# Performance work log

Measured on AMD Instinct MI355X. Metric: run time of the kernel, lower is better.

## Reference

```python
import jax, jax.numpy as jnp
import numpy as np

EPS = 1e-8  # torch.nn.CosineSimilarity default eps

def setup_inputs() -> dict:
    key = jax.random.key(0)
    k1, k2 = jax.random.split(key)
    B, R, T, D = 256, 36, 64, 1024
    img_feats = jax.random.normal(k1, (B, R, D), dtype=jnp.float32)
    cap_feats = jax.random.normal(k2, (B, T, D), dtype=jnp.float32)
    cap_mask = jnp.ones((B, T), dtype=jnp.float32)  # unused by the original forward
    return {"img_feats": img_feats, "cap_feats": cap_feats, "cap_mask": cap_mask}

def reference(img_feats, cap_feats, cap_mask):
    # img_feats: (B, R, D); cap_feats: (B, T, D)
    # cosine similarity between every region r and every caption word t:
    # scores[b, r, t] = (img[b,r] . cap[b,t]) / max(||img[b,r]|| * ||cap[b,t]||, eps)
    dots = jnp.einsum('brd,btd->brt', img_feats, cap_feats)
    img_norm = jnp.linalg.norm(img_feats, axis=-1)  # (B, R)
    cap_norm = jnp.linalg.norm(cap_feats, axis=-1)  # (B, T)
    denom = jnp.maximum(img_norm[:, :, None] * cap_norm[:, None, :], EPS)
    scores = dots / denom  # (B, R, T)
    # softmax over regions (dim=1 in the original)
    attn = jax.nn.softmax(scores, axis=1)  # (B, R, T)
    # weighted sum over regions -> per-word image representation (B, T, D)
    img_cap_reps = jnp.einsum('brt,brd->btd', attn, img_feats)
    return img_cap_reps
```

## Files before the change

### kernel.cpp

```cpp
#include <hip/hip_runtime.h>
#include <hip/hip_bf16.h>

#define DDIM 1024
#define RREG 36
#define TTOK 64
#define KPAD 48

typedef __attribute__((ext_vector_type(4))) float f32x4;
typedef __attribute__((ext_vector_type(8))) short bf16x8;

__device__ __forceinline__ float sq4(float4 v) {
  return v.x * v.x + v.y * v.y + v.z * v.z + v.w * v.w;
}

__device__ __forceinline__ bf16x8 cvt8(float4 a, float4 b) {
  union { bf16x8 v; __hip_bfloat162 h[4]; } u;
  u.h[0] = __float22bfloat162_rn(make_float2(a.x, a.y));
  u.h[1] = __float22bfloat162_rn(make_float2(a.z, a.w));
  u.h[2] = __float22bfloat162_rn(make_float2(b.x, b.y));
  u.h[3] = __float22bfloat162_rn(make_float2(b.z, b.w));
  return u.v;
}

__device__ __forceinline__ bf16x8 pack8(const float* v) {
  union { bf16x8 x; __hip_bfloat162 h[4]; } u;
#pragma unroll
  for (int i = 0; i < 4; ++i)
    u.h[i] = __float22bfloat162_rn(make_float2(v[2 * i], v[2 * i + 1]));
  return u.x;
}

__device__ __forceinline__ unsigned short f2bf(float x) {
  unsigned int u = __float_as_uint(x);
  u += 0x7fffu + ((u >> 16) & 1u);
  return (unsigned short)(u >> 16);
}

__global__ __launch_bounds__(192) void scan_attn(
    const float* __restrict__ img, const float* __restrict__ cap,
    unsigned short* __restrict__ attnw) {
  __shared__ float sdots[16][52];
  __shared__ float sni[KPAD];
  __shared__ float snc[16];

  const int tid  = threadIdx.x;
  const int lane = tid & 63;
  const int wave = tid >> 6;
  const int fm   = lane & 15;
  const int kq   = lane >> 4;
  const int b    = blockIdx.x >> 2;
  const int t0   = (blockIdx.x & 3) << 4;

  const float* capb = cap + (size_t)b * TTOK * DDIM;
  const float* imgb = img + (size_t)b * RREG * DDIM;

  const int t = t0 + fm;
  const int r = wave * 16 + fm;
  const bool rv = (r < RREG);

  const float* aptr = capb + t * DDIM + kq * 8;
  const float* bptr = imgb + (rv ? r : 0) * DDIM + kq * 8;

  f32x4 acc0 = {0.f, 0.f, 0.f, 0.f}, acc1 = {0.f, 0.f, 0.f, 0.f};
  float cn = 0.f, inrm = 0.f;

#pragma unroll 2
  for (int kc = 0; kc < 16; ++kc) {
    float4 a0 = *(const float4*)(aptr);
    float4 a1 = *(const float4*)(aptr + 4);
    float4 a2 = *(const float4*)(aptr + 32);
    float4 a3 = *(const float4*)(aptr + 36);
    float4 b0 = make_float4(0.f, 0.f, 0.f, 0.f), b1 = b0, b2 = b0, b3 = b0;
    if (rv) {
      b0 = *(const float4*)(bptr);
      b1 = *(const float4*)(bptr + 4);
      b2 = *(const float4*)(bptr + 32);
      b3 = *(const float4*)(bptr + 36);
    }
    aptr += 64; bptr += 64;
    cn   += sq4(a0) + sq4(a1) + sq4(a2) + sq4(a3);
    inrm += sq4(b0) + sq4(b1) + sq4(b2) + sq4(b3);
    acc0 = __builtin_amdgcn_mfma_f32_16x16x32_bf16(cvt8(a0, a1), cvt8(b0, b1), acc0, 0, 0, 0);
    acc1 = __builtin_amdgcn_mfma_f32_16x16x32_bf16(cvt8(a2, a3), cvt8(b2, b3), acc1, 0, 0, 0);
  }
  acc0 += acc1;

  cn   += __shfl_xor(cn, 16);   cn   += __shfl_xor(cn, 32);
  inrm += __shfl_xor(inrm, 16); inrm += __shfl_xor(inrm, 32);
  if (lane < 16) {
    sni[wave * 16 + fm] = sqrtf(inrm);
    if (wave == 0) snc[fm] = sqrtf(cn);
  }
#pragma unroll
  for (int i = 0; i < 4; ++i)
    sdots[kq * 4 + i][wave * 16 + fm] = acc0[i];
  __syncthreads();

  if (tid < 16) {
    const float cnv = snc[tid];
    float sc[RREG];
    float mx = -1e30f;
#pragma unroll
    for (int rr = 0; rr < RREG; ++rr) {
      float dnm = fmaxf(sni[rr] * cnv, 1e-8f);
      float v = sdots[tid][rr] / dnm;
      sc[rr] = v;
      mx = fmaxf(mx, v);
    }
    float sum = 0.f;
#pragma unroll
    for (int rr = 0; rr < RREG; ++rr) {
      float ev = __expf(sc[rr] - mx);
      sc[rr] = ev;
      sum += ev;
    }
    const float rinv = 1.f / sum;
    unsigned short* arow = attnw + ((size_t)b * TTOK + t0 + tid) * KPAD;
#pragma unroll
    for (int r0 = 0; r0 < RREG; r0 += 4) {
      ushort4 p;
      p.x = f2bf(sc[r0 + 0] * rinv);
      p.y = f2bf(sc[r0 + 1] * rinv);
      p.z = f2bf(sc[r0 + 2] * rinv);
      p.w = f2bf(sc[r0 + 3] * rinv);
      *(ushort4*)(arow + r0) = p;
    }
    ushort4 zz; zz.x = 0; zz.y = 0; zz.z = 0; zz.w = 0;
    *(ushort4*)(arow + 36) = zz;
    *(ushort4*)(arow + 40) = zz;
    *(ushort4*)(arow + 44) = zz;
  }
}

__global__ __launch_bounds__(256) void scan_out(
    const float* __restrict__ img, const unsigned short* __restrict__ attnw,
    float* __restrict__ out) {
  const int tid  = threadIdx.x;
  const int lane = tid & 63;
  const int wave = tid >> 6;
  const int fm   = lane & 15;
  const int kq   = lane >> 4;
  const int b    = blockIdx.x >> 2;
  const int d0   = (blockIdx.x & 3) << 8;

  const float* imgb = img + (size_t)b * RREG * DDIM;
  const unsigned short* attb = attnw + (size_t)b * TTOK * KPAD;
  float* outb = out + (size_t)b * TTOK * DDIM;

  const unsigned short* ap = attb + (wave * 16 + fm) * KPAD;
  bf16x8 zf = {0, 0, 0, 0, 0, 0, 0, 0};
  bf16x8 af0 = *(const bf16x8*)(ap + kq * 8);
  bf16x8 af1 = zf;
  if (kq < 2) af1 = *(const bf16x8*)(ap + 32 + kq * 8);

  for (int s = 0; s < 16; ++s) {
    const int d = d0 + s * 16 + fm;
    float v[8];
#pragma unroll
    for (int j = 0; j < 8; ++j) v[j] = imgb[(kq * 8 + j) * DDIM + d];
    bf16x8 bf0 = pack8(v);
    bf16x8 bf1 = zf;
    if (kq == 0) {
      float w[8];
#pragma unroll
      for (int j = 0; j < 4; ++j) w[j] = imgb[(32 + j) * DDIM + d];
#pragma unroll
      for (int j = 4; j < 8; ++j) w[j] = 0.f;
      bf1 = pack8(w);
    }
    f32x4 o = {0.f, 0.f, 0.f, 0.f};
    o = __builtin_amdgcn_mfma_f32_16x16x32_bf16(af0, bf0, o, 0, 0, 0);
    o = __builtin_amdgcn_mfma_f32_16x16x32_bf16(af1, bf1, o, 0, 0, 0);
    float* op = outb + (wave * 16 + kq * 4) * DDIM + d;
#pragma unroll
    for (int i = 0; i < 4; ++i) op[i * DDIM] = o[i];
  }
}

extern "C" void kernel_launch(void* const* d_in, const int* in_sizes, int n_in,
                              void* d_out, int out_size, void* d_ws, size_t ws_size,
                              hipStream_t stream) {
  const float* img = (const float*)d_in[0];
  const float* cap = (const float*)d_in[1];
  float* out = (float*)d_out;
  unsigned short* attnw = (unsigned short*)d_ws;

  scan_attn<<<dim3(1024), dim3(192), 0, stream>>>(img, cap, attnw);
  scan_out<<<dim3(1024), dim3(256), 0, stream>>>(img, attnw, out);
}
```

Measured before the change: 178.9 us.

## Stage cap and img chunks as bf16 in LDS before MFMA in scan_attn

The dot-product kernel now uses 256 threads that cooperatively load 256-column chunks of the 16 caption rows and 36 image rows as float4, convert them to bf16, and store them in padded shared memory. The first three waves then run MFMAs from LDS. Before, each lane streamed strided global loads directly into MFMA operands, which gave poor coalescing and had the padded image rows issue predicated loads. The new scheme adds LDS traffic and two barriers per chunk, and leaves one wave idle during the MFMA phase.

```diff
diff --git a/kernel.cpp b/kernel.cpp
--- a/kernel.cpp
+++ b/kernel.cpp
@@ -5,6 +5,8 @@
 #define RREG 36
 #define TTOK 64
 #define KPAD 48
+#define CHUNK 256
+#define LSTR 264
 
 typedef __attribute__((ext_vector_type(4))) float f32x4;
 typedef __attribute__((ext_vector_type(8))) short bf16x8;
@@ -13,13 +15,11 @@
   return v.x * v.x + v.y * v.y + v.z * v.z + v.w * v.w;
 }
 
-__device__ __forceinline__ bf16x8 cvt8(float4 a, float4 b) {
-  union { bf16x8 v; __hip_bfloat162 h[4]; } u;
-  u.h[0] = __float22bfloat162_rn(make_float2(a.x, a.y));
-  u.h[1] = __float22bfloat162_rn(make_float2(a.z, a.w));
-  u.h[2] = __float22bfloat162_rn(make_float2(b.x, b.y));
-  u.h[3] = __float22bfloat162_rn(make_float2(b.z, b.w));
-  return u.v;
+__device__ __forceinline__ ushort4 cvt4(float4 v) {
+  union { ushort4 u; __hip_bfloat162 h[2]; } r;
+  r.h[0] = __float22bfloat162_rn(make_float2(v.x, v.y));
+  r.h[1] = __float22bfloat162_rn(make_float2(v.z, v.w));
+  return r.u;
 }
 
 __device__ __forceinline__ bf16x8 pack8(const float* v) {
@@ -36,9 +36,11 @@
   return (unsigned short)(u >> 16);
 }
 
-__global__ __launch_bounds__(192) void scan_attn(
+__global__ __launch_bounds__(256) void scan_attn(
     const float* __restrict__ img, const float* __restrict__ cap,
     unsigned short* __restrict__ attnw) {
+  __shared__ unsigned short scap[16 * LSTR];
+  __shared__ unsigned short simg[48 * LSTR];
   __shared__ float sdots[16][52];
   __shared__ float sni[KPAD];
   __shared__ float snc[16];
@@ -54,46 +56,58 @@
   const float* capb = cap + (size_t)b * TTOK * DDIM;
   const float* imgb = img + (size_t)b * RREG * DDIM;
 
-  const int t = t0 + fm;
-  const int r = wave * 16 + fm;
-  const bool rv = (r < RREG);
-
-  const float* aptr = capb + t * DDIM + kq * 8;
-  const float* bptr = imgb + (rv ? r : 0) * DDIM + kq * 8;
-
-  f32x4 acc0 = {0.f, 0.f, 0.f, 0.f}, acc1 = {0.f, 0.f, 0.f, 0.f};
-  float cn = 0.f, inrm = 0.f;
-
-#pragma unroll 2
-  for (int kc = 0; kc < 16; ++kc) {
-    float4 a0 = *(const float4*)(aptr);
-    float4 a1 = *(const float4*)(aptr + 4);
-    float4 a2 = *(const float4*)(aptr + 32);
-    float4 a3 = *(const float4*)(aptr + 36);
-    float4 b0 = make_float4(0.f, 0.f, 0.f, 0.f), b1 = b0, b2 = b0, b3 = b0;
-    if (rv) {
-      b0 = *(const float4*)(bptr);
-      b1 = *(const float4*)(bptr + 4);
-      b2 = *(const float4*)(bptr + 32);
-      b3 = *(const float4*)(bptr + 36);
-    }
-    aptr += 64; bptr += 64;
-    cn   += sq4(a0) + sq4(a1) + sq4(a2) + sq4(a3);
-    inrm += sq4(b0) + sq4(b1) + sq4(b2) + sq4(b3);
-    acc0 = __builtin_amdgcn_mfma_f32_16x16x32_bf16(cvt8(a0, a1), cvt8(b0, b1), acc0, 0, 0, 0);
-    acc1 = __builtin_amdgcn_mfma_f32_16x16x32_bf16(cvt8(a2, a3), cvt8(b2, b3), acc1, 0, 0, 0);
-  }
-  acc0 += acc1;
-
-  cn   += __shfl_xor(cn, 16);   cn   += __shfl_xor(cn, 32);
-  inrm += __shfl_xor(inrm, 16); inrm += __shfl_xor(inrm, 32);
-  if (lane < 16) {
-    sni[wave * 16 + fm] = sqrtf(inrm);
-    if (wave == 0) snc[fm] = sqrtf(cn);
-  }
-#pragma unroll
-  for (int i = 0; i < 4; ++i)
-    sdots[kq * 4 + i][wave * 16 + fm] = acc0[i];
+  {
+    ushort4 zz; zz.x = 0; zz.y = 0; zz.z = 0; zz.w = 0;
+    for (int i = tid; i < 792; i += 256)
+      *(ushort4*)(simg + 36 * LSTR + i * 4) = zz;
+  }
+
+  const int u = tid >> 2;
+  const int q = tid & 3;
+  const bool active = (u < 52);
+  const bool is_cap = (u < 16);
+  const float* srcrow = is_cap ? (capb + (size_t)(t0 + u) * DDIM)
+                               : (imgb + (size_t)(active ? (u - 16) : 0) * DDIM);
+  unsigned short* dstrow = is_cap ? (scap + u * LSTR) : (simg + (u - 16) * LSTR);
+
+  float nrm = 0.f;
+  f32x4 acc = {0.f, 0.f, 0.f, 0.f};
+
+  for (int c = 0; c < 4; ++c) {
+    if (c) __syncthreads();
+    if (active) {
+#pragma unroll
+      for (int s = 0; s < 16; ++s) {
+        const int col = s * 16 + q * 4;
+        float4 v = *(const float4*)(srcrow + c * CHUNK + col);
+        nrm += sq4(v);
+        *(ushort4*)(dstrow + col) = cvt4(v);
+      }
+    }
+    __syncthreads();
+    if (wave < 3) {
+      const unsigned short* arow = scap + fm * LSTR + kq * 8;
+      const unsigned short* brow = simg + (wave * 16 + fm) * LSTR + kq * 8;
+#pragma unroll
+      for (int ks = 0; ks < 8; ++ks) {
+        bf16x8 av = *(const bf16x8*)(arow + ks * 32);
+        bf16x8 bv = *(const bf16x8*)(brow + ks * 32);
+        acc = __builtin_amdgcn_mfma_f32_16x16x32_bf16(av, bv, acc, 0, 0, 0);
+      }
+    }
+  }
+
+  nrm += __shfl_xor(nrm, 1);
+  nrm += __shfl_xor(nrm, 2);
+  if (active && q == 0) {
+    if (is_cap) snc[u] = sqrtf(nrm);
+    else        sni[u - 16] = sqrtf(nrm);
+  }
+  if (wave < 3) {
+#pragma unroll
+    for (int i = 0; i < 4; ++i)
+      sdots[kq * 4 + i][wave * 16 + fm] = acc[i];
+  }
   __syncthreads();
 
   if (tid < 16) {
@@ -185,6 +199,6 @@
   float* out = (float*)d_out;
   unsigned short* attnw = (unsigned short*)d_ws;
 
-  scan_attn<<<dim3(1024), dim3(192), 0, stream>>>(img, cap, attnw);
+  scan_attn<<<dim3(1024), dim3(256), 0, stream>>>(img, cap, attnw);
   scan_out<<<dim3(1024), dim3(256), 0, stream>>>(img, attnw, out);
 }
```

After: 170.1 us. 4.9% less time.

## Restructure scan_attn to one block per batch with split-K across eight waves

Applied to the files above, without the earlier changes.

The attention kernel now processes a whole batch per 512-thread block. Each of eight waves computes all 64x36 dot products over its own 128-wide slice of D and handles the full token and region tiles. Partial results are reduced through shared memory, and norms are reduced across waves. This removes the reloading of img rows by four separate blocks and the redundant cap and img norm computations, and it raises per-wave MFMA work. In exchange the grid shrinks to 256 blocks, shared memory use grows to about 53KB, and register pressure from 12 accumulators rises.

```diff
diff --git a/kernel.cpp b/kernel.cpp
--- a/kernel.cpp
+++ b/kernel.cpp
@@ -5,6 +5,7 @@
 #define RREG 36
 #define TTOK 64
 #define KPAD 48
+#define SLOTSTR 49
 
 typedef __attribute__((ext_vector_type(4))) float f32x4;
 typedef __attribute__((ext_vector_type(8))) short bf16x8;
@@ -36,86 +37,162 @@
   return (unsigned short)(u >> 16);
 }
 
-__global__ __launch_bounds__(192) void scan_attn(
+__global__ __launch_bounds__(512) void scan_attn(
     const float* __restrict__ img, const float* __restrict__ cap,
     unsigned short* __restrict__ attnw) {
-  __shared__ float sdots[16][52];
-  __shared__ float sni[KPAD];
-  __shared__ float snc[16];
+  __shared__ __align__(16) unsigned char smem[53760];
+  float* pdots = (float*)smem;
+  float* snc_p = (float*)(smem + 50176);
+  float* sni_p = (float*)(smem + 52224);
 
   const int tid  = threadIdx.x;
   const int lane = tid & 63;
-  const int wave = tid >> 6;
+  const int w    = tid >> 6;
   const int fm   = lane & 15;
   const int kq   = lane >> 4;
-  const int b    = blockIdx.x >> 2;
-  const int t0   = (blockIdx.x & 3) << 4;
+  const int b    = blockIdx.x;
 
   const float* capb = cap + (size_t)b * TTOK * DDIM;
   const float* imgb = img + (size_t)b * RREG * DDIM;
 
-  const int t = t0 + fm;
-  const int r = wave * 16 + fm;
-  const bool rv = (r < RREG);
-
-  const float* aptr = capb + t * DDIM + kq * 8;
-  const float* bptr = imgb + (rv ? r : 0) * DDIM + kq * 8;
-
-  f32x4 acc0 = {0.f, 0.f, 0.f, 0.f}, acc1 = {0.f, 0.f, 0.f, 0.f};
-  float cn = 0.f, inrm = 0.f;
-
-#pragma unroll 2
-  for (int kc = 0; kc < 16; ++kc) {
-    float4 a0 = *(const float4*)(aptr);
-    float4 a1 = *(const float4*)(aptr + 4);
-    float4 a2 = *(const float4*)(aptr + 32);
-    float4 a3 = *(const float4*)(aptr + 36);
-    float4 b0 = make_float4(0.f, 0.f, 0.f, 0.f), b1 = b0, b2 = b0, b3 = b0;
-    if (rv) {
-      b0 = *(const float4*)(bptr);
-      b1 = *(const float4*)(bptr + 4);
-      b2 = *(const float4*)(bptr + 32);
-      b3 = *(const float4*)(bptr + 36);
-    }
-    aptr += 64; bptr += 64;
-    cn   += sq4(a0) + sq4(a1) + sq4(a2) + sq4(a3);
-    inrm += sq4(b0) + sq4(b1) + sq4(b2) + sq4(b3);
-    acc0 = __builtin_amdgcn_mfma_f32_16x16x32_bf16(cvt8(a0, a1), cvt8(b0, b1), acc0, 0, 0, 0);
-    acc1 = __builtin_amdgcn_mfma_f32_16x16x32_bf16(cvt8(a2, a3), cvt8(b2, b3), acc1, 0, 0, 0);
-  }
-  acc0 += acc1;
-
-  cn   += __shfl_xor(cn, 16);   cn   += __shfl_xor(cn, 32);
-  inrm += __shfl_xor(inrm, 16); inrm += __shfl_xor(inrm, 32);
+  const float* capk = capb + w * 128 + kq * 8;
+  const float* imgk = imgb + w * 128 + kq * 8;
+
+  f32x4 acc[4][3];
+#pragma unroll
+  for (int tt = 0; tt < 4; ++tt)
+#pragma unroll
+    for (int rt = 0; rt < 3; ++rt) acc[tt][rt] = (f32x4){0.f, 0.f, 0.f, 0.f};
+  float cnp[4] = {0.f, 0.f, 0.f, 0.f};
+  float inp[3] = {0.f, 0.f, 0.f};
+
+  const int  r2  = 32 + fm;
+  const bool r2v = (r2 < RREG);
+
+#pragma unroll
+  for (int ks = 0; ks < 4; ++ks) {
+    const int ko = ks * 32;
+    float4 a0[4], a1[4];
+#pragma unroll
+    for (int tt = 0; tt < 4; ++tt) {
+      const float* p = capk + (tt * 16 + fm) * DDIM + ko;
+      a0[tt] = *(const float4*)p;
+      a1[tt] = *(const float4*)(p + 4);
+    }
+    float4 b0[3], b1[3];
+#pragma unroll
+    for (int rt = 0; rt < 2; ++rt) {
+      const float* p = imgk + (rt * 16 + fm) * DDIM + ko;
+      b0[rt] = *(const float4*)p;
+      b1[rt] = *(const float4*)(p + 4);
+    }
+    {
+      const float* p = imgk + (r2v ? r2 : 0) * DDIM + ko;
+      float4 t0 = *(const float4*)p;
+      float4 t1 = *(const float4*)(p + 4);
+      if (!r2v) { t0 = make_float4(0.f, 0.f, 0.f, 0.f); t1 = t0; }
+      b0[2] = t0; b1[2] = t1;
+    }
+#pragma unroll
+    for (int tt = 0; tt < 4; ++tt) cnp[tt] += sq4(a0[tt]) + sq4(a1[tt]);
+#pragma unroll
+    for (int rt = 0; rt < 3; ++rt) inp[rt] += sq4(b0[rt]) + sq4(b1[rt]);
+    bf16x8 af[4], bfv[3];
+#pragma unroll
+    for (int tt = 0; tt < 4; ++tt) af[tt] = cvt8(a0[tt], a1[tt]);
+#pragma unroll
+    for (int rt = 0; rt < 3; ++rt) bfv[rt] = cvt8(b0[rt], b1[rt]);
+#pragma unroll
+    for (int tt = 0; tt < 4; ++tt)
+#pragma unroll
+      for (int rt = 0; rt < 3; ++rt)
+        acc[tt][rt] = __builtin_amdgcn_mfma_f32_16x16x32_bf16(af[tt], bfv[rt], acc[tt][rt], 0, 0, 0);
+  }
+
+#pragma unroll
+  for (int tt = 0; tt < 4; ++tt) {
+    cnp[tt] += __shfl_xor(cnp[tt], 16);
+    cnp[tt] += __shfl_xor(cnp[tt], 32);
+  }
+#pragma unroll
+  for (int rt = 0; rt < 3; ++rt) {
+    inp[rt] += __shfl_xor(inp[rt], 16);
+    inp[rt] += __shfl_xor(inp[rt], 32);
+  }
   if (lane < 16) {
-    sni[wave * 16 + fm] = sqrtf(inrm);
-    if (wave == 0) snc[fm] = sqrtf(cn);
-  }
-#pragma unroll
-  for (int i = 0; i < 4; ++i)
-    sdots[kq * 4 + i][wave * 16 + fm] = acc0[i];
+#pragma unroll
+    for (int tt = 0; tt < 4; ++tt) snc_p[w * 64 + tt * 16 + lane] = cnp[tt];
+#pragma unroll
+    for (int rt = 0; rt < 3; ++rt) {
+      int r = rt * 16 + lane;
+      if (r < RREG) sni_p[w * 48 + r] = inp[rt];
+    }
+  }
+
+  float* slot = pdots + (w & 3) * (TTOK * SLOTSTR);
+  if (w < 4) {
+#pragma unroll
+    for (int tt = 0; tt < 4; ++tt)
+#pragma unroll
+      for (int rt = 0; rt < 3; ++rt)
+#pragma unroll
+        for (int i = 0; i < 4; ++i)
+          slot[(tt * 16 + kq * 4 + i) * SLOTSTR + rt * 16 + fm] = acc[tt][rt][i];
+  }
   __syncthreads();
-
-  if (tid < 16) {
-    const float cnv = snc[tid];
+  if (w >= 4) {
+#pragma unroll
+    for (int tt = 0; tt < 4; ++tt)
+#pragma unroll
+      for (int rt = 0; rt < 3; ++rt)
+#pragma unroll
+        for (int i = 0; i < 4; ++i) {
+          int idx = (tt * 16 + kq * 4 + i) * SLOTSTR + rt * 16 + fm;
+          slot[idx] += acc[tt][rt][i];
+        }
+  }
+  __syncthreads();
+
+  if (tid < 64) {
+    float s = 0.f;
+#pragma unroll
+    for (int w2 = 0; w2 < 8; ++w2) s += snc_p[w2 * 64 + tid];
+    snc_p[tid] = sqrtf(s);
+  } else if (tid < 112) {
+    int r = tid - 64;
+    if (r < RREG) {
+      float s = 0.f;
+#pragma unroll
+      for (int w2 = 0; w2 < 8; ++w2) s += sni_p[w2 * 48 + r];
+      sni_p[r] = sqrtf(s);
+    }
+  }
+  __syncthreads();
+
+  if (w < 4 && lane < 16) {
+    const int t = w * 16 + lane;
+    const float nc = snc_p[t];
     float sc[RREG];
     float mx = -1e30f;
 #pragma unroll
-    for (int rr = 0; rr < RREG; ++rr) {
-      float dnm = fmaxf(sni[rr] * cnv, 1e-8f);
-      float v = sdots[tid][rr] / dnm;
-      sc[rr] = v;
+    for (int r = 0; r < RREG; ++r) {
+      float d = pdots[t * SLOTSTR + r] +
+                pdots[TTOK * SLOTSTR + t * SLOTSTR + r] +
+                pdots[2 * TTOK * SLOTSTR + t * SLOTSTR + r] +
+                pdots[3 * TTOK * SLOTSTR + t * SLOTSTR + r];
+      float v = d / fmaxf(sni_p[r] * nc, 1e-8f);
+      sc[r] = v;
       mx = fmaxf(mx, v);
     }
     float sum = 0.f;
 #pragma unroll
-    for (int rr = 0; rr < RREG; ++rr) {
-      float ev = __expf(sc[rr] - mx);
-      sc[rr] = ev;
+    for (int r = 0; r < RREG; ++r) {
+      float ev = __expf(sc[r] - mx);
+      sc[r] = ev;
       sum += ev;
     }
     const float rinv = 1.f / sum;
-    unsigned short* arow = attnw + ((size_t)b * TTOK + t0 + tid) * KPAD;
+    unsigned short* arow = attnw + ((size_t)b * TTOK + t) * KPAD;
 #pragma unroll
     for (int r0 = 0; r0 < RREG; r0 += 4) {
       ushort4 p;
@@ -161,12 +238,12 @@
     bf16x8 bf0 = pack8(v);
     bf16x8 bf1 = zf;
     if (kq == 0) {
-      float w[8];
-#pragma unroll
-      for (int j = 0; j < 4; ++j) w[j] = imgb[(32 + j) * DDIM + d];
-#pragma unroll
-      for (int j = 4; j < 8; ++j) w[j] = 0.f;
-      bf1 = pack8(w);
+      float wv[8];
+#pragma unroll
+      for (int j = 0; j < 4; ++j) wv[j] = imgb[(32 + j) * DDIM + d];
+#pragma unroll
+      for (int j = 4; j < 8; ++j) wv[j] = 0.f;
+      bf1 = pack8(wv);
     }
     f32x4 o = {0.f, 0.f, 0.f, 0.f};
     o = __builtin_amdgcn_mfma_f32_16x16x32_bf16(af0, bf0, o, 0, 0, 0);
@@ -185,6 +262,6 @@
   float* out = (float*)d_out;
   unsigned short* attnw = (unsigned short*)d_ws;
 
-  scan_attn<<<dim3(1024), dim3(192), 0, stream>>>(img, cap, attnw);
+  scan_attn<<<dim3(256), dim3(512), 0, stream>>>(img, cap, attnw);
   scan_out<<<dim3(1024), dim3(256), 0, stream>>>(img, attnw, out);
 }
```

New measurement: 177.6 us. About the same (-0.7%).

## Restructure attention kernel as warp-specialized LDS double-buffered pipeline per batch

Applied to the files above, without the earlier changes.

The score kernel now runs one block per batch with 8 waves. Four producer waves stream caption and image chunks into double-buffered LDS using global_load_lds, and four consumer waves convert those chunks to bf16 and issue MFMAs over all 36 regions. Each image row is now read once per batch instead of once per token group, and the global load latency is overlapped with compute. The output kernel is split across twice as many blocks, each covering half the D range. In exchange there are only 256 score blocks, half of the waves do no MFMA work, and correctness depends on the hand-written waitcnt and barrier scheme.

```diff
diff --git a/kernel.cpp b/kernel.cpp
--- a/kernel.cpp
+++ b/kernel.cpp
@@ -5,30 +5,11 @@
 #define RREG 36
 #define TTOK 64
 #define KPAD 48
+#define QSTR 1032
+#define BUFB (28 * QSTR)
 
 typedef __attribute__((ext_vector_type(4))) float f32x4;
 typedef __attribute__((ext_vector_type(8))) short bf16x8;
-
-__device__ __forceinline__ float sq4(float4 v) {
-  return v.x * v.x + v.y * v.y + v.z * v.z + v.w * v.w;
-}
-
-__device__ __forceinline__ bf16x8 cvt8(float4 a, float4 b) {
-  union { bf16x8 v; __hip_bfloat162 h[4]; } u;
-  u.h[0] = __float22bfloat162_rn(make_float2(a.x, a.y));
-  u.h[1] = __float22bfloat162_rn(make_float2(a.z, a.w));
-  u.h[2] = __float22bfloat162_rn(make_float2(b.x, b.y));
-  u.h[3] = __float22bfloat162_rn(make_float2(b.z, b.w));
-  return u.v;
-}
-
-__device__ __forceinline__ bf16x8 pack8(const float* v) {
-  union { bf16x8 x; __hip_bfloat162 h[4]; } u;
-#pragma unroll
-  for (int i = 0; i < 4; ++i)
-    u.h[i] = __float22bfloat162_rn(make_float2(v[2 * i], v[2 * i + 1]));
-  return u.x;
-}
 
 __device__ __forceinline__ unsigned short f2bf(float x) {
   unsigned int u = __float_as_uint(x);
@@ -36,86 +17,157 @@
   return (unsigned short)(u >> 16);
 }
 
-__global__ __launch_bounds__(192) void scan_attn(
+__device__ __forceinline__ bf16x8 pack8(const float* v) {
+  union { bf16x8 x; __hip_bfloat162 h[4]; } u;
+#pragma unroll
+  for (int i = 0; i < 4; ++i)
+    u.h[i] = __float22bfloat162_rn(make_float2(v[2 * i], v[2 * i + 1]));
+  return u.x;
+}
+
+__device__ __forceinline__ bf16x8 lds_frag(const unsigned char* p, float& nsq, bool do_n) {
+  float2 v0 = *(const float2*)(p);
+  float2 v1 = *(const float2*)(p + 8);
+  float2 v2 = *(const float2*)(p + 16);
+  float2 v3 = *(const float2*)(p + 24);
+  if (do_n)
+    nsq += v0.x * v0.x + v0.y * v0.y + v1.x * v1.x + v1.y * v1.y +
+           v2.x * v2.x + v2.y * v2.y + v3.x * v3.x + v3.y * v3.y;
+  union { bf16x8 v; __hip_bfloat162 h[4]; } u;
+  u.h[0] = __float22bfloat162_rn(v0);
+  u.h[1] = __float22bfloat162_rn(v1);
+  u.h[2] = __float22bfloat162_rn(v2);
+  u.h[3] = __float22bfloat162_rn(v3);
+  return u.v;
+}
+
+__global__ __launch_bounds__(512, 2) void scan_attn(
     const float* __restrict__ img, const float* __restrict__ cap,
     unsigned short* __restrict__ attnw) {
-  __shared__ float sdots[16][52];
-  __shared__ float sni[KPAD];
-  __shared__ float snc[16];
+  __shared__ __align__(16) unsigned char smem[2 * BUFB];
 
   const int tid  = threadIdx.x;
   const int lane = tid & 63;
   const int wave = tid >> 6;
   const int fm   = lane & 15;
   const int kq   = lane >> 4;
-  const int b    = blockIdx.x >> 2;
-  const int t0   = (blockIdx.x & 3) << 4;
+  const int b    = blockIdx.x;
 
   const float* capb = cap + (size_t)b * TTOK * DDIM;
   const float* imgb = img + (size_t)b * RREG * DDIM;
 
-  const int t = t0 + fm;
-  const int r = wave * 16 + fm;
-  const bool rv = (r < RREG);
-
-  const float* aptr = capb + t * DDIM + kq * 8;
-  const float* bptr = imgb + (rv ? r : 0) * DDIM + kq * 8;
-
-  f32x4 acc0 = {0.f, 0.f, 0.f, 0.f}, acc1 = {0.f, 0.f, 0.f, 0.f};
-  float cn = 0.f, inrm = 0.f;
+  for (int i = tid; i < 1548; i += 512) {
+    int bs = (i >= 774);
+    *(unsigned int*)(smem + bs * BUFB + 25 * QSTR + (size_t)(i - bs * 774) * 4) = 0u;
+  }
+
+  const bool producer = (wave >= 4);
+  const int  pw = wave & 3;
+  const int  lrow = lane >> 4;
+  const int  lcol = (lane & 15) * 16;
+
+  auto issue = [&](int c) {
+    unsigned char* lbuf = smem + (size_t)(c & 1) * BUFB;
+    const int colb = c * 256;
+    for (int qd = pw; qd < 25; qd += 4) {
+      const char* g;
+      if (qd < 16) g = (const char*)(capb + (size_t)(qd * 4 + lrow) * DDIM) + colb + lcol;
+      else         g = (const char*)(imgb + (size_t)((qd - 16) * 4 + lrow) * DDIM) + colb + lcol;
+      __builtin_amdgcn_global_load_lds(
+          (const __attribute__((address_space(1))) void*)g,
+          (__attribute__((address_space(3))) void*)(lbuf + (size_t)qd * QSTR),
+          16, 0, 0);
+    }
+  };
+
+  if (producer) {
+    issue(0);
+    issue(1);
+    asm volatile("s_waitcnt vmcnt(6)" ::: "memory");
+  }
+  asm volatile("s_waitcnt lgkmcnt(0)" ::: "memory");
+  asm volatile("s_barrier" ::: "memory");
+
+  f32x4 acc0 = {0.f, 0.f, 0.f, 0.f};
+  f32x4 acc1 = {0.f, 0.f, 0.f, 0.f};
+  f32x4 acc2 = {0.f, 0.f, 0.f, 0.f};
+  float cn = 0.f, in0 = 0.f, in1 = 0.f, in2 = 0.f;
+
+  const int arow = wave * 16 + fm;
+  const int aoff = (arow >> 2) * QSTR + (arow & 3) * 256;
+  const int boff0 = 16 * QSTR + (fm >> 2) * QSTR + (fm & 3) * 256;
+  const int boff1 = 16 * QSTR + ((16 + fm) >> 2) * QSTR + ((16 + fm) & 3) * 256;
+  const int boff2 = 16 * QSTR + ((32 + fm) >> 2) * QSTR + ((32 + fm) & 3) * 256;
 
 #pragma unroll 2
-  for (int kc = 0; kc < 16; ++kc) {
-    float4 a0 = *(const float4*)(aptr);
-    float4 a1 = *(const float4*)(aptr + 4);
-    float4 a2 = *(const float4*)(aptr + 32);
-    float4 a3 = *(const float4*)(aptr + 36);
-    float4 b0 = make_float4(0.f, 0.f, 0.f, 0.f), b1 = b0, b2 = b0, b3 = b0;
-    if (rv) {
-      b0 = *(const float4*)(bptr);
-      b1 = *(const float4*)(bptr + 4);
-      b2 = *(const float4*)(bptr + 32);
-      b3 = *(const float4*)(bptr + 36);
-    }
-    aptr += 64; bptr += 64;
-    cn   += sq4(a0) + sq4(a1) + sq4(a2) + sq4(a3);
-    inrm += sq4(b0) + sq4(b1) + sq4(b2) + sq4(b3);
-    acc0 = __builtin_amdgcn_mfma_f32_16x16x32_bf16(cvt8(a0, a1), cvt8(b0, b1), acc0, 0, 0, 0);
-    acc1 = __builtin_amdgcn_mfma_f32_16x16x32_bf16(cvt8(a2, a3), cvt8(b2, b3), acc1, 0, 0, 0);
-  }
-  acc0 += acc1;
-
-  cn   += __shfl_xor(cn, 16);   cn   += __shfl_xor(cn, 32);
-  inrm += __shfl_xor(inrm, 16); inrm += __shfl_xor(inrm, 32);
-  if (lane < 16) {
-    sni[wave * 16 + fm] = sqrtf(inrm);
-    if (wave == 0) snc[fm] = sqrtf(cn);
-  }
-#pragma unroll
-  for (int i = 0; i < 4; ++i)
-    sdots[kq * 4 + i][wave * 16 + fm] = acc0[i];
-  __syncthreads();
-
-  if (tid < 16) {
-    const float cnv = snc[tid];
+  for (int c = 0; c < 16; ++c) {
+    if (!producer) {
+      const unsigned char* buf = smem + (size_t)(c & 1) * BUFB;
+#pragma unroll
+      for (int ks = 0; ks < 2; ++ks) {
+        const int ko = ks * 128 + kq * 32;
+        bf16x8 af = lds_frag(buf + aoff + ko, cn, true);
+        bf16x8 f0 = lds_frag(buf + boff0 + ko, in0, wave == 0);
+        bf16x8 f1 = lds_frag(buf + boff1 + ko, in1, wave == 0);
+        bf16x8 f2 = lds_frag(buf + boff2 + ko, in2, wave == 0);
+        acc0 = __builtin_amdgcn_mfma_f32_16x16x32_bf16(af, f0, acc0, 0, 0, 0);
+        acc1 = __builtin_amdgcn_mfma_f32_16x16x32_bf16(af, f1, acc1, 0, 0, 0);
+        acc2 = __builtin_amdgcn_mfma_f32_16x16x32_bf16(af, f2, acc2, 0, 0, 0);
+      }
+    }
+    asm volatile("s_waitcnt lgkmcnt(0)" ::: "memory");
+    asm volatile("s_barrier" ::: "memory");
+    if (producer) {
+      if (c + 2 < 16) issue(c + 2);
+      asm volatile("s_waitcnt vmcnt(6)" ::: "memory");
+    }
+    asm volatile("s_barrier" ::: "memory");
+  }
+
+  cn  += __shfl_xor(cn, 16);  cn  += __shfl_xor(cn, 32);
+  in0 += __shfl_xor(in0, 16); in0 += __shfl_xor(in0, 32);
+  in1 += __shfl_xor(in1, 16); in1 += __shfl_xor(in1, 32);
+  in2 += __shfl_xor(in2, 16); in2 += __shfl_xor(in2, 32);
+
+  float* sdots = (float*)smem;
+  float* snc   = (float*)(smem + 13312);
+  float* sni   = (float*)(smem + 13568);
+  if (!producer) {
+    if (lane < 16) snc[wave * 16 + fm] = cn;
+    if (wave == 0 && lane < 16) {
+      sni[fm] = in0; sni[16 + fm] = in1; sni[32 + fm] = in2;
+    }
+#pragma unroll
+    for (int i = 0; i < 4; ++i) {
+      float* dp = sdots + (size_t)(wave * 16 + kq * 4 + i) * 52;
+      dp[fm]      = acc0[i];
+      dp[16 + fm] = acc1[i];
+      dp[32 + fm] = acc2[i];
+    }
+  }
+  asm volatile("s_waitcnt lgkmcnt(0)" ::: "memory");
+  asm volatile("s_barrier" ::: "memory");
+
+  if (wave < 4 && lane < 16) {
+    const int t = wave * 16 + lane;
+    const float nc = sqrtf(snc[t]);
     float sc[RREG];
     float mx = -1e30f;
 #pragma unroll
-    for (int rr = 0; rr < RREG; ++rr) {
-      float dnm = fmaxf(sni[rr] * cnv, 1e-8f);
-      float v = sdots[tid][rr] / dnm;
-      sc[rr] = v;
+    for (int r = 0; r < RREG; ++r) {
+      float v = sdots[(size_t)t * 52 + r] / fmaxf(sqrtf(sni[r]) * nc, 1e-8f);
+      sc[r] = v;
       mx = fmaxf(mx, v);
     }
     float sum = 0.f;
 #pragma unroll
-    for (int rr = 0; rr < RREG; ++rr) {
-      float ev = __expf(sc[rr] - mx);
-      sc[rr] = ev;
+    for (int r = 0; r < RREG; ++r) {
+      float ev = __expf(sc[r] - mx);
+      sc[r] = ev;
       sum += ev;
     }
     const float rinv = 1.f / sum;
-    unsigned short* arow = attnw + ((size_t)b * TTOK + t0 + tid) * KPAD;
+    unsigned short* arw = attnw + ((size_t)b * TTOK + t) * KPAD;
 #pragma unroll
     for (int r0 = 0; r0 < RREG; r0 += 4) {
       ushort4 p;
@@ -123,12 +175,12 @@
       p.y = f2bf(sc[r0 + 1] * rinv);
       p.z = f2bf(sc[r0 + 2] * rinv);
       p.w = f2bf(sc[r0 + 3] * rinv);
-      *(ushort4*)(arow + r0) = p;
+      *(ushort4*)(arw + r0) = p;
     }
     ushort4 zz; zz.x = 0; zz.y = 0; zz.z = 0; zz.w = 0;
-    *(ushort4*)(arow + 36) = zz;
-    *(ushort4*)(arow + 40) = zz;
-    *(ushort4*)(arow + 44) = zz;
+    *(ushort4*)(arw + 36) = zz;
+    *(ushort4*)(arw + 40) = zz;
+    *(ushort4*)(arw + 44) = zz;
   }
 }
 
@@ -140,8 +192,8 @@
   const int wave = tid >> 6;
   const int fm   = lane & 15;
   const int kq   = lane >> 4;
-  const int b    = blockIdx.x >> 2;
-  const int d0   = (blockIdx.x & 3) << 8;
+  const int b    = blockIdx.x >> 3;
+  const int d0   = (blockIdx.x & 7) << 7;
 
   const float* imgb = img + (size_t)b * RREG * DDIM;
   const unsigned short* attb = attnw + (size_t)b * TTOK * KPAD;
@@ -153,7 +205,7 @@
   bf16x8 af1 = zf;
   if (kq < 2) af1 = *(const bf16x8*)(ap + 32 + kq * 8);
 
-  for (int s = 0; s < 16; ++s) {
+  for (int s = 0; s < 8; ++s) {
     const int d = d0 + s * 16 + fm;
     float v[8];
 #pragma unroll
@@ -161,12 +213,12 @@
     bf16x8 bf0 = pack8(v);
     bf16x8 bf1 = zf;
     if (kq == 0) {
-      float w[8];
-#pragma unroll
-      for (int j = 0; j < 4; ++j) w[j] = imgb[(32 + j) * DDIM + d];
-#pragma unroll
-      for (int j = 4; j < 8; ++j) w[j] = 0.f;
-      bf1 = pack8(w);
+      float wv[8];
+#pragma unroll
+      for (int j = 0; j < 4; ++j) wv[j] = imgb[(32 + j) * DDIM + d];
+#pragma unroll
+      for (int j = 4; j < 8; ++j) wv[j] = 0.f;
+      bf1 = pack8(wv);
     }
     f32x4 o = {0.f, 0.f, 0.f, 0.f};
     o = __builtin_amdgcn_mfma_f32_16x16x32_bf16(af0, bf0, o, 0, 0, 0);
@@ -185,6 +237,6 @@
   float* out = (float*)d_out;
   unsigned short* attnw = (unsigned short*)d_ws;
 
-  scan_attn<<<dim3(1024), dim3(192), 0, stream>>>(img, cap, attnw);
-  scan_out<<<dim3(1024), dim3(256), 0, stream>>>(img, attnw, out);
-}
+  scan_attn<<<dim3(256), dim3(512), 0, stream>>>(img, cap, attnw);
+  scan_out<<<dim3(2048), dim3(256), 0, stream>>>(img, attnw, out);
+}
```

Result: faster. 167.6 us (-6.3%).
